# Kernel tuning notes

Hardware: AMD Instinct MI355X
Metric: run time of the kernel (lower is better)

Reference implementation:

```python
import jax, jax.numpy as jnp
import numpy as np

B, T, D, KDIM = 256, 512, 256, 256

def setup_inputs() -> dict:
    key = jax.random.key(0)
    k1, k2, k3 = jax.random.split(key, 3)
    inputs = jax.random.normal(k1, (B, T, D), dtype=jnp.float32)
    # glorot-style scaling for stability of the recurrence
    U = jax.random.normal(k2, (D, KDIM), dtype=jnp.float32) * (1.0 / np.sqrt(D))
    W = jax.random.normal(k3, (KDIM, KDIM), dtype=jnp.float32) * (1.0 / np.sqrt(KDIM))
    b = jnp.zeros((KDIM,), dtype=jnp.float32)
    return {"inputs": inputs, "U": U, "W": W, "b": b}

def reference(inputs, U, W, b):
    # vanilla RNN: h_t = tanh(x_t U + h_{t-1} W + b); returns final hidden state
    xU = jnp.einsum('btd,dk->btk', inputs, U) + b  # precompute input projection [B,T,K]

    def step(h, xu_t):
        h = jnp.tanh(xu_t + h @ W)
        return h, None

    h0 = jnp.zeros((inputs.shape[0], W.shape[0]), dtype=inputs.dtype)
    h_final, _ = jax.lax.scan(step, h0, jnp.swapaxes(xU, 0, 1))  # scan over time
    # original keras code keeps a singleton time axis on the state: [B,1,K]
    return h_final[:, None, :]
```

## Files before the change

### kernel.cpp

```cpp
#include <hip/hip_runtime.h>
#include <hip/hip_bf16.h>


typedef _Float16 half8_t __attribute__((ext_vector_type(8)));
typedef _Float16 half2_t __attribute__((ext_vector_type(2)));
typedef float    float4_t __attribute__((ext_vector_type(4)));

#define MFMA16(a, b, c) __builtin_amdgcn_mfma_f32_16x16x32_f16((a), (b), (c), 0, 0, 0)
#define BARRIER_LGKM() asm volatile("s_waitcnt lgkmcnt(0)\n\ts_barrier" ::: "memory")

__device__ __forceinline__ half2_t pk_h2(float a, float b) {
    auto r = __builtin_amdgcn_cvt_pkrtz(a, b);
    return __builtin_bit_cast(half2_t, r);
}

__device__ __forceinline__ float fast_tanh(float x) {
    float e = __expf(2.0f * x);
    return 1.0f - 2.0f * __builtin_amdgcn_rcpf(e + 1.0f);
}

__global__ void transpose_u(const float* __restrict__ U, _Float16* __restrict__ Ut) {
    int id = blockIdx.x * 256 + threadIdx.x;
    int d = id >> 8, n = id & 255;
    Ut[n * 264 + d] = (_Float16)U[id];
}

__global__ __launch_bounds__(256, 2) void xu_gemm(
    const float* __restrict__ x,
    const _Float16* __restrict__ Ut,
    half2_t* __restrict__ xu)
{
    const int tid = threadIdx.x;
    const int lane = tid & 63, w = tid >> 6, l15 = lane & 15, q = lane >> 4;
    const int bx = blockIdx.x;
    const int b = bx >> 5;
    const int t0 = ((bx >> 1) & 15) * 32;
    const int ch = bx & 1;
    const int rowg = w & 1, colg = w >> 1;
    const int n0 = ch * 128 + colg * 64;

    half8_t bf[2][2][8];
#pragma unroll
    for (int s = 0; s < 2; ++s)
#pragma unroll
        for (int tt = 0; tt < 2; ++tt) {
            const char* bp = (const char*)Ut
                           + (size_t)(n0 + 32 * s + 2 * l15 + tt) * 528 + q * 16;
#pragma unroll
            for (int c = 0; c < 8; ++c)
                bf[s][tt][c] = *(const half8_t*)(bp + c * 64);
        }

    const float* ap = x + ((size_t)b * 512 + t0 + 16 * rowg + l15) * 256 + 8 * q;
    half8_t af[8];
#pragma unroll
    for (int c = 0; c < 8; ++c) {
        float4 a0 = *(const float4*)(ap + 32 * c);
        float4 a1 = *(const float4*)(ap + 32 * c + 4);
        uint4 u;
        u.x = __builtin_bit_cast(unsigned, pk_h2(a0.x, a0.y));
        u.y = __builtin_bit_cast(unsigned, pk_h2(a0.z, a0.w));
        u.z = __builtin_bit_cast(unsigned, pk_h2(a1.x, a1.y));
        u.w = __builtin_bit_cast(unsigned, pk_h2(a1.z, a1.w));
        af[c] = __builtin_bit_cast(half8_t, u);
    }

    float4_t acc[2][2];
#pragma unroll
    for (int s = 0; s < 2; ++s)
#pragma unroll
        for (int tt = 0; tt < 2; ++tt)
#pragma unroll
            for (int i = 0; i < 4; ++i) acc[s][tt][i] = 0.f;

#pragma unroll
    for (int c = 0; c < 8; ++c)
#pragma unroll
        for (int s = 0; s < 2; ++s)
#pragma unroll
            for (int tt = 0; tt < 2; ++tt)
                acc[s][tt] = MFMA16(af[c], bf[s][tt][c], acc[s][tt]);

#pragma unroll
    for (int s = 0; s < 2; ++s)
#pragma unroll
        for (int i = 0; i < 4; ++i) {
            half2_t p = pk_h2(acc[s][0][i], acc[s][1][i]);
            xu[(size_t)((t0 + 16 * rowg + 4 * q + i) * 256 + b) * 128
               + (n0 >> 1) + 16 * s + l15] = p;
        }
}

__global__ __launch_bounds__(512, 2) void rnn_scan(
    const half2_t* __restrict__ xu,
    const float* __restrict__ W,
    const float* __restrict__ bias,
    float* __restrict__ out)
{
    __shared__ char lds[16896];
    const int tid = threadIdx.x;
    const int lane = tid & 63, w = tid >> 6, l15 = lane & 15, q = lane >> 4;
    const int blk = blockIdx.x;
    const int c0 = 32 * w + 2 * l15;

    half8_t wf[2][8];
#pragma unroll
    for (int tt = 0; tt < 2; ++tt)
#pragma unroll
        for (int c = 0; c < 8; ++c) {
            half8_t f;
#pragma unroll
            for (int j = 0; j < 8; ++j) {
                int k = 32 * c + q * 8 + j;
                f[j] = (_Float16)W[k * 256 + c0 + tt];
            }
            wf[tt][c] = f;
        }
    const float b0 = bias[c0], b1 = bias[c0 + 1];

    for (int i = tid; i < 16896 / 4; i += 512) ((int*)lds)[i] = 0;

    const int rowg0 = 16 * blk + 4 * q;
    const int cp = 16 * w + l15;

    auto load_xu = [&](half2_t (&dst)[4], int t) {
#pragma unroll
        for (int i = 0; i < 4; ++i)
            dst[i] = xu[((size_t)t * 256 + rowg0 + i) * 128 + cp];
    };

    half2_t xc[4], xn[4];
    load_xu(xc, 0);
    load_xu(xn, 1);
    __syncthreads();

    char* const hbuf0 = (char*)lds;
    char* const hbuf1 = (char*)lds + 8448;

    auto step = [&](half2_t (&xreg)[4], int t) {
        float4_t acc0, acc1;
#pragma unroll
        for (int i = 0; i < 4; ++i) {
            acc0[i] = (float)xreg[i][0];
            acc1[i] = (float)xreg[i][1];
        }

        int tp = t + 2 > 511 ? 511 : t + 2;
        load_xu(xreg, tp);

        const char* hcur = (t & 1) ? hbuf1 : hbuf0;
        half8_t af[8];
#pragma unroll
        for (int c = 0; c < 8; ++c)
            af[c] = *(const half8_t*)(hcur + l15 * 528 + c * 64 + q * 16);

#pragma unroll
        for (int c = 0; c < 8; ++c) {
            acc0 = MFMA16(af[c], wf[0][c], acc0);
            acc1 = MFMA16(af[c], wf[1][c], acc1);
        }

        if (t == 511) {
#pragma unroll
            for (int i = 0; i < 4; ++i) {
                float v0 = fast_tanh(acc0[i] + b0);
                float v1 = fast_tanh(acc1[i] + b1);
                float2 st; st.x = v0; st.y = v1;
                *(float2*)(&out[(rowg0 + i) * 256 + c0]) = st;
            }
        } else {
            char* hnext = ((t + 1) & 1) ? hbuf1 : hbuf0;
#pragma unroll
            for (int i = 0; i < 4; ++i) {
                float v0 = fast_tanh(acc0[i] + b0);
                float v1 = fast_tanh(acc1[i] + b1);
                *(half2_t*)(hnext + (4 * q + i) * 528 + c0 * 2) = pk_h2(v0, v1);
            }
            BARRIER_LGKM();
        }
    };

    for (int t2 = 0; t2 < 512; t2 += 2) {
        step(xc, t2);
        step(xn, t2 + 1);
    }
}

extern "C" void kernel_launch(void* const* d_in, const int* in_sizes, int n_in,
                              void* d_out, int out_size, void* d_ws, size_t ws_size,
                              hipStream_t stream) {
    const float* x = (const float*)d_in[0];
    const float* U = (const float*)d_in[1];
    const float* W = (const float*)d_in[2];
    const float* b = (const float*)d_in[3];
    float* out = (float*)d_out;

    char* ws = (char*)d_ws;
    _Float16* Ut = (_Float16*)ws;
    half2_t*  xu = (half2_t*)(ws + 262144);

    transpose_u<<<256, 256, 0, stream>>>(U, Ut);
    xu_gemm<<<8192, 256, 0, stream>>>(x, Ut, xu);
    rnn_scan<<<16, 512, 0, stream>>>(xu, W, b, out);
}
```

Measured before the change: 627.9 us.

## Restructure input-projection GEMM into LDS-tiled 64x256 blocks with swizzled shared memory

Result: faster. 573.0 us (-8.7%).

```diff
diff --git a/kernel.cpp b/kernel.cpp
--- a/kernel.cpp
+++ b/kernel.cpp
@@ -12,6 +12,9 @@
 __device__ __forceinline__ half2_t pk_h2(float a, float b) {
     auto r = __builtin_amdgcn_cvt_pkrtz(a, b);
     return __builtin_bit_cast(half2_t, r);
+}
+__device__ __forceinline__ unsigned pk_u(float a, float b) {
+    return __builtin_bit_cast(unsigned, pk_h2(a, b));
 }
 
 __device__ __forceinline__ float fast_tanh(float x) {
@@ -25,70 +28,112 @@
     Ut[n * 264 + d] = (_Float16)U[id];
 }
 
-__global__ __launch_bounds__(256, 2) void xu_gemm(
+__global__ __launch_bounds__(512, 1) void xu_gemm(
     const float* __restrict__ x,
     const _Float16* __restrict__ Ut,
     half2_t* __restrict__ xu)
 {
+    __shared__ char As[32768];
+    __shared__ char Bs[32768];
     const int tid = threadIdx.x;
     const int lane = tid & 63, w = tid >> 6, l15 = lane & 15, q = lane >> 4;
     const int bx = blockIdx.x;
-    const int b = bx >> 5;
-    const int t0 = ((bx >> 1) & 15) * 32;
-    const int ch = bx & 1;
+    const int b = bx >> 3, tc = bx & 7;
     const int rowg = w & 1, colg = w >> 1;
-    const int n0 = ch * 128 + colg * 64;
-
-    half8_t bf[2][2][8];
-#pragma unroll
-    for (int s = 0; s < 2; ++s)
-#pragma unroll
-        for (int tt = 0; tt < 2; ++tt) {
-            const char* bp = (const char*)Ut
-                           + (size_t)(n0 + 32 * s + 2 * l15 + tt) * 528 + q * 16;
-#pragma unroll
-            for (int c = 0; c < 8; ++c)
-                bf[s][tt][c] = *(const half8_t*)(bp + c * 64);
-        }
-
-    const float* ap = x + ((size_t)b * 512 + t0 + 16 * rowg + l15) * 256 + 8 * q;
-    half8_t af[8];
-#pragma unroll
-    for (int c = 0; c < 8; ++c) {
-        float4 a0 = *(const float4*)(ap + 32 * c);
-        float4 a1 = *(const float4*)(ap + 32 * c + 4);
+
+#pragma unroll
+    for (int i = 0; i < 4; ++i) {
+        int task = tid + 512 * i;
+        int r = task >> 5, ch = task & 31;
+        const float* gp = x + ((size_t)b * 512 + 64 * tc + r) * 256 + ch * 8;
+        float4 a0 = *(const float4*)gp;
+        float4 a1 = *(const float4*)(gp + 4);
         uint4 u;
-        u.x = __builtin_bit_cast(unsigned, pk_h2(a0.x, a0.y));
-        u.y = __builtin_bit_cast(unsigned, pk_h2(a0.z, a0.w));
-        u.z = __builtin_bit_cast(unsigned, pk_h2(a1.x, a1.y));
-        u.w = __builtin_bit_cast(unsigned, pk_h2(a1.z, a1.w));
-        af[c] = __builtin_bit_cast(half8_t, u);
+        u.x = pk_u(a0.x, a0.y);
+        u.y = pk_u(a0.z, a0.w);
+        u.z = pk_u(a1.x, a1.y);
+        u.w = pk_u(a1.z, a1.w);
+        *(uint4*)(As + r * 512 + (ch ^ (r & 7)) * 16) = u;
     }
 
-    float4_t acc[2][2];
-#pragma unroll
-    for (int s = 0; s < 2; ++s)
-#pragma unroll
-        for (int tt = 0; tt < 2; ++tt)
-#pragma unroll
-            for (int i = 0; i < 4; ++i) acc[s][tt][i] = 0.f;
-
-#pragma unroll
-    for (int c = 0; c < 8; ++c)
-#pragma unroll
-        for (int s = 0; s < 2; ++s)
+    uint4 breg[4];
+    auto loadBq = [&](int qtr) {
+#pragma unroll
+        for (int i = 0; i < 4; ++i) {
+            int task = tid + 512 * i;
+            int n = task >> 3, ch = task & 7;
+            breg[i] = *(const uint4*)((const char*)Ut + (size_t)n * 528
+                                      + qtr * 128 + ch * 16);
+        }
+    };
+    auto writeBq = [&]() {
+#pragma unroll
+        for (int i = 0; i < 4; ++i) {
+            int task = tid + 512 * i;
+            int n = task >> 3, ch = task & 7;
+            *(uint4*)(Bs + n * 128 + (ch ^ ((n >> 1) & 7)) * 16) = breg[i];
+        }
+    };
+
+    float4_t acc[2][2][2];
+#pragma unroll
+    for (int rt = 0; rt < 2; ++rt)
+#pragma unroll
+        for (int sp = 0; sp < 2; ++sp)
 #pragma unroll
             for (int tt = 0; tt < 2; ++tt)
-                acc[s][tt] = MFMA16(af[c], bf[s][tt][c], acc[s][tt]);
-
-#pragma unroll
-    for (int s = 0; s < 2; ++s)
-#pragma unroll
-        for (int i = 0; i < 4; ++i) {
-            half2_t p = pk_h2(acc[s][0][i], acc[s][1][i]);
-            xu[(size_t)((t0 + 16 * rowg + 4 * q + i) * 256 + b) * 128
-               + (n0 >> 1) + 16 * s + l15] = p;
-        }
+#pragma unroll
+                for (int i = 0; i < 4; ++i) acc[rt][sp][tt][i] = 0.f;
+
+    loadBq(0);
+    writeBq();
+    __syncthreads();
+
+    for (int qtr = 0; qtr < 4; ++qtr) {
+        if (qtr < 3) loadBq(qtr + 1);
+#pragma unroll
+        for (int c = 0; c < 2; ++c) {
+            half8_t af[2], bf[2][2];
+#pragma unroll
+            for (int rt = 0; rt < 2; ++rt) {
+                int r = 32 * rowg + 16 * rt + l15;
+                int ch = qtr * 8 + c * 4 + q;
+                af[rt] = *(const half8_t*)(As + r * 512 + (ch ^ (r & 7)) * 16);
+            }
+#pragma unroll
+            for (int sp = 0; sp < 2; ++sp)
+#pragma unroll
+                for (int tt = 0; tt < 2; ++tt) {
+                    int n = 64 * colg + 32 * sp + 2 * l15 + tt;
+                    int ch = c * 4 + q;
+                    bf[sp][tt] = *(const half8_t*)(Bs + n * 128
+                                                   + (ch ^ ((n >> 1) & 7)) * 16);
+                }
+#pragma unroll
+            for (int rt = 0; rt < 2; ++rt)
+#pragma unroll
+                for (int sp = 0; sp < 2; ++sp)
+#pragma unroll
+                    for (int tt = 0; tt < 2; ++tt)
+                        acc[rt][sp][tt] = MFMA16(af[rt], bf[sp][tt], acc[rt][sp][tt]);
+        }
+        if (qtr < 3) {
+            __syncthreads();
+            writeBq();
+            __syncthreads();
+        }
+    }
+
+#pragma unroll
+    for (int rt = 0; rt < 2; ++rt)
+#pragma unroll
+        for (int sp = 0; sp < 2; ++sp)
+#pragma unroll
+            for (int i = 0; i < 4; ++i) {
+                int t = 64 * tc + 32 * rowg + 16 * rt + 4 * q + i;
+                half2_t p = pk_h2(acc[rt][sp][0][i], acc[rt][sp][1][i]);
+                xu[((size_t)t * 256 + b) * 128 + 32 * colg + 16 * sp + l15] = p;
+            }
 }
 
 __global__ __launch_bounds__(512, 2) void rnn_scan(
@@ -145,8 +190,7 @@
             acc1[i] = (float)xreg[i][1];
         }
 
-        int tp = t + 2 > 511 ? 511 : t + 2;
-        load_xu(xreg, tp);
+        load_xu(xreg, (t + 2) & 511);
 
         const char* hcur = (t & 1) ? hbuf1 : hbuf0;
         half8_t af[8];
@@ -200,6 +244,6 @@
     half2_t*  xu = (half2_t*)(ws + 262144);
 
     transpose_u<<<256, 256, 0, stream>>>(U, Ut);
-    xu_gemm<<<8192, 256, 0, stream>>>(x, Ut, xu);
+    xu_gemm<<<2048, 512, 0, stream>>>(x, Ut, xu);
     rnn_scan<<<16, 512, 0, stream>>>(xu, W, b, out);
 }
```
